# Kernel tuning notes

Measured on AMD Instinct MI355X. Metric: run time of the kernel, lower is better.

Reference implementation:

```python
import jax, jax.numpy as jnp
import numpy as np


def setup_inputs() -> dict:
    key = jax.random.key(0)
    k1, k2 = jax.random.split(key)
    B, C, H, W = 8, 19, 512, 512
    pred = jax.random.normal(k1, (B, C, H, W), dtype=jnp.float32)
    target = jax.random.randint(k2, (B, H, W), 0, C)
    return {"pred": pred, "target": target}


def reference(pred, target):
    B, C, H, W = pred.shape
    N = H * W
    p = jax.nn.softmax(pred, axis=1).reshape(B, C, N)                      # [B,C,N]
    # one-hot float target per class: target_flat = (target == c).float()
    tgt = (target.reshape(B, 1, N) == jnp.arange(C)[None, :, None]).astype(p.dtype)  # [B,C,N]
    signs = 2.0 * tgt - 1.0
    errors = 1.0 - p * signs                                               # [B,C,N]
    # descending sort of errors; permutation applied to the target too
    perm = jnp.argsort(-errors, axis=-1)                                   # [B,C,N]
    errors_sorted = jnp.take_along_axis(errors, perm, axis=-1)
    gt_sorted = jnp.take_along_axis(tgt, perm, axis=-1)
    # Lovasz gradient (Jaccard extension gradient)
    gts = jnp.sum(gt_sorted, axis=-1, keepdims=True)                       # [B,C,1]
    intersection = gts - jnp.cumsum(gt_sorted, axis=-1)
    union = gts + jnp.cumsum(1.0 - gt_sorted, axis=-1)
    jaccard = 1.0 - intersection / union
    grad = jnp.concatenate([jaccard[..., :1], jaccard[..., 1:] - jaccard[..., :-1]], axis=-1)
    # dot(relu(errors_sorted), grad) per (b,c), then mean over B*C
    loss_bc = jnp.sum(jax.nn.relu(errors_sorted) * grad, axis=-1)          # [B,C]
    return jnp.sum(loss_bc) / (B * C)
```

## Files before the change

### kernel.cpp

```cpp
#include <hip/hip_runtime.h>

#define BATCH 8
#define NCLS  19
#define LOGN  18
#define NPIX  (1u << LOGN)
#define NB    64
#define BLK1  512
#define HCOPY 8
#define HSTR  (NCLS * NB + 4)

template<int BPB>
__global__ __launch_bounds__(BLK1, 8) void k_hist(
    const float* __restrict__ pred, const int* __restrict__ target,
    unsigned short* __restrict__ hist_part, float* __restrict__ s2_part,
    unsigned short* __restrict__ cnt_part)
{
    constexpr int PPB = (int)(NPIX / BPB);
    constexpr int PXT = PPB / BLK1;

    __shared__ unsigned hist[HCOPY * HSTR];
    __shared__ float    s2lds[NCLS];
    __shared__ unsigned cntlds[NCLS];

    const int b     = blockIdx.x / BPB;
    const int chunk = blockIdx.x % BPB;
    const int tid   = threadIdx.x;
    const int lane  = tid & 63;

    unsigned* hpar = hist + (lane & (HCOPY - 1)) * HSTR;

    for (int i = tid; i < HCOPY * HSTR; i += BLK1) hist[i] = 0u;
    if (tid < NCLS) { s2lds[tid] = 0.f; cntlds[tid] = 0u; }
    __syncthreads();

    const float* pb = pred + (((size_t)b * NCLS) << LOGN);
    const int*   tb = target + ((size_t)b << LOGN);

    #pragma unroll 1
    for (int it = 0; it < PXT; ++it) {
        const int n  = chunk * PPB + it * BLK1 + tid;
        const int tg = tb[n];

        float e[NCLS];
        float s = 0.f;
        #pragma unroll
        for (int c = 0; c < NCLS; ++c) {
            e[c] = __expf(pb[((size_t)c << LOGN) + n]);
            s += e[c];
        }
        const float r = __builtin_amdgcn_rcpf(s) * (float)NB;

        float et = 0.f;
        #pragma unroll
        for (int c = 0; c < NCLS; ++c) {
            const float t = e[c] * r;
            int bin = (int)t; bin = bin > NB - 1 ? NB - 1 : bin;
            et = (c == tg) ? e[c] : et;
            if (c != tg && bin != 0) atomicAdd(&hpar[c * NB + bin], 1u);
        }
        atomicAdd(&s2lds[tg], fmaf(et * r, -1.0f / (float)NB, 1.0f));
        atomicAdd(&cntlds[tg], 1u);
    }
    __syncthreads();

    for (int i = tid; i < NCLS * NB; i += BLK1) {
        unsigned v = 0;
        #pragma unroll
        for (int k = 0; k < HCOPY; ++k) v += hist[k * HSTR + i];
        const int c = i >> 6, bin = i & (NB - 1);
        hist_part[((size_t)(b * NCLS + c) * BPB + chunk) * NB + bin] = (unsigned short)v;
    }
    if (tid < NCLS) {
        s2_part [(size_t)(b * NCLS + tid) * BPB + chunk] = s2lds[tid];
        cnt_part[(size_t)(b * NCLS + tid) * BPB + chunk] = (unsigned short)cntlds[tid];
    }
}

template<int BPB>
__global__ __launch_bounds__(256) void k_finish(
    const unsigned short* __restrict__ hist_part, const float* __restrict__ s2_part,
    const unsigned short* __restrict__ cnt_part, float* __restrict__ loss_bc)
{
    __shared__ unsigned hsum[4][NB];
    __shared__ float s2tot, nctot;

    const int bc   = blockIdx.x;
    const int tid  = threadIdx.x;
    const int lane = tid & 63;
    const int w    = tid >> 6;

    const unsigned short* hp = hist_part + (size_t)bc * BPB * NB;
    unsigned h = 0;
    #pragma unroll 1
    for (int k = 0; k < BPB / 4; ++k)
        h += hp[(size_t)(w * (BPB / 4) + k) * NB + lane];
    hsum[w][lane] = h;

    if (w == 1) {
        float v = 0.f;
        for (int k = lane; k < BPB; k += 64) v += s2_part[(size_t)bc * BPB + k];
        #pragma unroll
        for (int off = 32; off > 0; off >>= 1) v += __shfl_down(v, off, 64);
        if (lane == 0) s2tot = v;
    }
    if (w == 2) {
        unsigned v = 0;
        for (int k = lane; k < BPB; k += 64) v += cnt_part[(size_t)bc * BPB + k];
        #pragma unroll
        for (int off = 32; off > 0; off >>= 1) v += __shfl_down(v, off, 64);
        if (lane == 0) nctot = (float)v;
    }
    __syncthreads();

    if (w == 0) {
        const unsigned hb = hsum[0][lane] + hsum[1][lane] + hsum[2][lane] + hsum[3][lane];
        const unsigned hrev = __shfl(hb, 63 - lane, 64);
        unsigned sc = hrev;
        #pragma unroll
        for (int off = 1; off < 64; off <<= 1) {
            const unsigned v = __shfl_up(sc, off, 64);
            if (lane >= off) sc += v;
        }
        const float ncf = nctot;
        const float Nf  = (float)NPIX;
        const float Mf  = Nf - ncf;
        const unsigned Rab = sc - hrev;
        float fRh = (float)sc;
        if (lane == 63) fRh = Mf;
        const float gR  = (Rab > 0)   ? (float)Rab / ((float)Rab + ncf) : 0.0f;
        const float gRh = (fRh > 0.f) ? fRh / (fRh + ncf) : 0.0f;
        float red = gR + gRh;
        #pragma unroll
        for (int off = 32; off > 0; off >>= 1) red += __shfl_down(red, off, 64);
        if (lane == 0)
            loss_bc[bc] = Mf / Nf + red * (0.5f / (float)NB) + s2tot / Nf;
    }
}

__global__ __launch_bounds__(256) void k_reduce(
    const float* __restrict__ loss_bc, float* __restrict__ out)
{
    __shared__ float r[256];
    const int tid = threadIdx.x;
    r[tid] = (tid < BATCH * NCLS) ? loss_bc[tid] : 0.0f;
    __syncthreads();
    for (int off = 128; off > 0; off >>= 1) {
        if (tid < off) r[tid] += r[tid + off];
        __syncthreads();
    }
    if (tid == 0) out[0] = r[0] * (1.0f / (float)(BATCH * NCLS));
}

template<int BPB>
static void launch_all(const float* pred, const int* target, unsigned char* ws,
                       float* out, hipStream_t stream)
{
    unsigned short* hist_part = (unsigned short*)ws;
    size_t off = (size_t)BATCH * NCLS * BPB * NB * sizeof(unsigned short);
    float* s2_part = (float*)(ws + off);
    off += (size_t)BATCH * NCLS * BPB * sizeof(float);
    unsigned short* cnt_part = (unsigned short*)(ws + off);
    off += (size_t)BATCH * NCLS * BPB * sizeof(unsigned short);
    float* loss_bc = (float*)(ws + off);

    hipLaunchKernelGGL(k_hist<BPB>,   dim3(BATCH * BPB),  dim3(BLK1), 0, stream,
                       pred, target, hist_part, s2_part, cnt_part);
    hipLaunchKernelGGL(k_finish<BPB>, dim3(BATCH * NCLS), dim3(256),  0, stream,
                       hist_part, s2_part, cnt_part, loss_bc);
    hipLaunchKernelGGL(k_reduce,      dim3(1),            dim3(256),  0, stream,
                       loss_bc, out);
}

extern "C" void kernel_launch(void* const* d_in, const int* in_sizes, int n_in,
                              void* d_out, int out_size, void* d_ws, size_t ws_size,
                              hipStream_t stream)
{
    const float* pred   = (const float*)d_in[0];
    const int*   target = (const int*)d_in[1];
    float*       out    = (float*)d_out;
    unsigned char* ws   = (unsigned char*)d_ws;

    auto need = [](int bpb) {
        return (size_t)BATCH * NCLS * bpb * (NB * sizeof(unsigned short)
                                             + sizeof(float) + sizeof(unsigned short))
             + (size_t)BATCH * NCLS * sizeof(float);
    };

    if (ws_size >= need(128))     launch_all<128>(pred, target, ws, out, stream);
    else                          launch_all<64>(pred, target, ws, out, stream);
}
```

Before: 44.77 us.

## Double-buffer pred/target tiles into LDS via async global_load_lds with fewer blocks

The histogram kernel now copies each 512-pixel tile of all 19 class planes, plus the matching target values, into LDS using asynchronous global-to-LDS loads. The next tile is prefetched while the current one is being processed, and a barrier closes each iteration. The grid shrinks to 32 chunks per batch, 256 blocks in total, and the template-selected 128/64 chunk variants are removed. The goal is to hide global memory latency through explicit prefetching rather than through high occupancy. The cost is about 120KB of LDS per block, which allows only one block per CU, plus a barrier on every tile and a dependence on the async loads completing before that barrier.

```diff
diff --git a/kernel.cpp b/kernel.cpp
--- a/kernel.cpp
+++ b/kernel.cpp
@@ -6,73 +6,102 @@
 #define NPIX  (1u << LOGN)
 #define NB    64
 #define BLK1  512
+#define CPB   32
+#define PPBLK (NPIX / CPB)
+#define TPX   512
+#define NT    (PPBLK / TPX)
 #define HCOPY 8
 #define HSTR  (NCLS * NB + 4)
 
-template<int BPB>
-__global__ __launch_bounds__(BLK1, 8) void k_hist(
+__device__ __forceinline__ void gload16(const void* g, void* l) {
+    __builtin_amdgcn_global_load_lds(
+        (const __attribute__((address_space(1))) unsigned*)g,
+        (__attribute__((address_space(3))) unsigned*)l, 16, 0, 0);
+}
+
+__global__ __launch_bounds__(BLK1) void k_hist(
     const float* __restrict__ pred, const int* __restrict__ target,
     unsigned short* __restrict__ hist_part, float* __restrict__ s2_part,
     unsigned short* __restrict__ cnt_part)
 {
-    constexpr int PPB = (int)(NPIX / BPB);
-    constexpr int PXT = PPB / BLK1;
-
+    __shared__ __align__(16) float pbuf[2][NCLS * TPX];
+    __shared__ __align__(16) int   tbuf[2][TPX];
     __shared__ unsigned hist[HCOPY * HSTR];
     __shared__ float    s2lds[NCLS];
     __shared__ unsigned cntlds[NCLS];
 
-    const int b     = blockIdx.x / BPB;
-    const int chunk = blockIdx.x % BPB;
+    const int b     = blockIdx.x / CPB;
+    const int chunk = blockIdx.x % CPB;
     const int tid   = threadIdx.x;
     const int lane  = tid & 63;
+    const int wid   = tid >> 6;
 
     unsigned* hpar = hist + (lane & (HCOPY - 1)) * HSTR;
 
     for (int i = tid; i < HCOPY * HSTR; i += BLK1) hist[i] = 0u;
     if (tid < NCLS) { s2lds[tid] = 0.f; cntlds[tid] = 0u; }
+
+    const float* pb = pred + (((size_t)b * NCLS) << LOGN) + (size_t)chunk * PPBLK;
+    const int*   tb = target + ((size_t)b << LOGN) + (size_t)chunk * PPBLK;
+
+    auto stage = [&](int buf, int t) {
+        const int px0 = t * TPX;
+        #pragma unroll
+        for (int j = 0; j < 5; ++j) {
+            const int i = wid * 5 + j;
+            if (i < 2 * NCLS) {
+                const int c = i >> 1, half = i & 1;
+                gload16(pb + ((size_t)c << LOGN) + px0 + half * 256 + lane * 4,
+                        &pbuf[buf][c * TPX + half * 256]);
+            } else if (i < 2 * NCLS + 2) {
+                const int hh = i - 2 * NCLS;
+                gload16(tb + px0 + hh * 256 + lane * 4, &tbuf[buf][hh * 256]);
+            }
+        }
+    };
+
+    stage(0, 0);
     __syncthreads();
 
-    const float* pb = pred + (((size_t)b * NCLS) << LOGN);
-    const int*   tb = target + ((size_t)b << LOGN);
-
     #pragma unroll 1
-    for (int it = 0; it < PXT; ++it) {
-        const int n  = chunk * PPB + it * BLK1 + tid;
-        const int tg = tb[n];
+    for (int t = 0; t < NT; ++t) {
+        const int cur = t & 1;
+        if (t + 1 < NT) stage(cur ^ 1, t + 1);
 
         float e[NCLS];
         float s = 0.f;
         #pragma unroll
         for (int c = 0; c < NCLS; ++c) {
-            e[c] = __expf(pb[((size_t)c << LOGN) + n]);
+            e[c] = __expf(pbuf[cur][c * TPX + tid]);
             s += e[c];
         }
-        const float r = __builtin_amdgcn_rcpf(s) * (float)NB;
+        const int   tg = tbuf[cur][tid];
+        const float r  = __builtin_amdgcn_rcpf(s) * (float)NB;
 
         float et = 0.f;
         #pragma unroll
         for (int c = 0; c < NCLS; ++c) {
-            const float t = e[c] * r;
-            int bin = (int)t; bin = bin > NB - 1 ? NB - 1 : bin;
+            const float tt = e[c] * r;
+            int bin = (int)tt; bin = bin > NB - 1 ? NB - 1 : bin;
             et = (c == tg) ? e[c] : et;
             if (c != tg && bin != 0) atomicAdd(&hpar[c * NB + bin], 1u);
         }
         atomicAdd(&s2lds[tg], fmaf(et * r, -1.0f / (float)NB, 1.0f));
         atomicAdd(&cntlds[tg], 1u);
-    }
-    __syncthreads();
+
+        __syncthreads();
+    }
 
     for (int i = tid; i < NCLS * NB; i += BLK1) {
         unsigned v = 0;
         #pragma unroll
         for (int k = 0; k < HCOPY; ++k) v += hist[k * HSTR + i];
         const int c = i >> 6, bin = i & (NB - 1);
-        hist_part[((size_t)(b * NCLS + c) * BPB + chunk) * NB + bin] = (unsigned short)v;
+        hist_part[((size_t)(b * NCLS + c) * CPB + chunk) * NB + bin] = (unsigned short)v;
     }
     if (tid < NCLS) {
-        s2_part [(size_t)(b * NCLS + tid) * BPB + chunk] = s2lds[tid];
-        cnt_part[(size_t)(b * NCLS + tid) * BPB + chunk] = (unsigned short)cntlds[tid];
+        s2_part [(size_t)(b * NCLS + tid) * CPB + chunk] = s2lds[tid];
+        cnt_part[(size_t)(b * NCLS + tid) * CPB + chunk] = (unsigned short)cntlds[tid];
     }
 }
 
@@ -151,26 +180,6 @@
     if (tid == 0) out[0] = r[0] * (1.0f / (float)(BATCH * NCLS));
 }
 
-template<int BPB>
-static void launch_all(const float* pred, const int* target, unsigned char* ws,
-                       float* out, hipStream_t stream)
-{
-    unsigned short* hist_part = (unsigned short*)ws;
-    size_t off = (size_t)BATCH * NCLS * BPB * NB * sizeof(unsigned short);
-    float* s2_part = (float*)(ws + off);
-    off += (size_t)BATCH * NCLS * BPB * sizeof(float);
-    unsigned short* cnt_part = (unsigned short*)(ws + off);
-    off += (size_t)BATCH * NCLS * BPB * sizeof(unsigned short);
-    float* loss_bc = (float*)(ws + off);
-
-    hipLaunchKernelGGL(k_hist<BPB>,   dim3(BATCH * BPB),  dim3(BLK1), 0, stream,
-                       pred, target, hist_part, s2_part, cnt_part);
-    hipLaunchKernelGGL(k_finish<BPB>, dim3(BATCH * NCLS), dim3(256),  0, stream,
-                       hist_part, s2_part, cnt_part, loss_bc);
-    hipLaunchKernelGGL(k_reduce,      dim3(1),            dim3(256),  0, stream,
-                       loss_bc, out);
-}
-
 extern "C" void kernel_launch(void* const* d_in, const int* in_sizes, int n_in,
                               void* d_out, int out_size, void* d_ws, size_t ws_size,
                               hipStream_t stream)
@@ -180,12 +189,18 @@
     float*       out    = (float*)d_out;
     unsigned char* ws   = (unsigned char*)d_ws;
 
-    auto need = [](int bpb) {
-        return (size_t)BATCH * NCLS * bpb * (NB * sizeof(unsigned short)
-                                             + sizeof(float) + sizeof(unsigned short))
-             + (size_t)BATCH * NCLS * sizeof(float);
-    };
-
-    if (ws_size >= need(128))     launch_all<128>(pred, target, ws, out, stream);
-    else                          launch_all<64>(pred, target, ws, out, stream);
-}
+    unsigned short* hist_part = (unsigned short*)ws;
+    size_t off = (size_t)BATCH * NCLS * CPB * NB * sizeof(unsigned short);
+    float* s2_part = (float*)(ws + off);
+    off += (size_t)BATCH * NCLS * CPB * sizeof(float);
+    unsigned short* cnt_part = (unsigned short*)(ws + off);
+    off += (size_t)BATCH * NCLS * CPB * sizeof(unsigned short);
+    float* loss_bc = (float*)(ws + off);
+
+    hipLaunchKernelGGL(k_hist,        dim3(BATCH * CPB),  dim3(BLK1), 0, stream,
+                       pred, target, hist_part, s2_part, cnt_part);
+    hipLaunchKernelGGL(k_finish<CPB>, dim3(BATCH * NCLS), dim3(256),  0, stream,
+                       hist_part, s2_part, cnt_part, loss_bc);
+    hipLaunchKernelGGL(k_reduce,      dim3(1),            dim3(256),  0, stream,
+                       loss_bc, out);
+}
```

Result: slower. 55.73 us (+24.5%).
